# Performance work log

Hardware: AMD Instinct MI355X
Metric: run time of the kernel (lower is better)

The kernel has to match this reference:

```python
import jax, jax.numpy as jnp
import numpy as np

DIM, HEADS, HEAD_DIM, P = 256, 8, 64, 16
N = P * P          # 256 tokens
H2 = HEADS // 2    # heads in SDPA branch
SCALE = HEAD_DIM ** -0.5
BN_EPS = 1e-5


def _depthwise(x, w, kh, kw):
    # x: (b, DIM, P, P), w: (DIM, kh*kw) depthwise kernel -> same spatial size
    rhs = w.reshape(DIM, 1, kh, kw)
    return jax.lax.conv_general_dilated(
        x, rhs, window_strides=(1, 1),
        padding=((kh // 2, kh // 2), (kw // 2, kw // 2)),
        dimension_numbers=('NCHW', 'OIHW', 'NCHW'),
        feature_group_count=DIM)


def setup_inputs() -> dict:
    key = jax.random.key(0)
    ks = jax.random.split(key, 8)
    b = 128
    return {
        'x': jax.random.normal(ks[0], (b, N, DIM), jnp.float32),
        'bn_gamma': jax.random.uniform(ks[1], (DIM,), jnp.float32, 0.5, 1.5),
        'bn_beta': jax.random.normal(ks[2], (DIM,), jnp.float32) * 0.1,
        'bn_mean': jax.random.normal(ks[3], (DIM,), jnp.float32) * 0.1,
        'bn_var': jax.random.uniform(ks[4], (DIM,), jnp.float32, 0.5, 1.5),
        'w_qkv': jax.random.normal(ks[5], (DIM, 6), jnp.float32) * 0.1,
        'w_qs': jax.random.normal(ks[6], (DIM, 3), jnp.float32) * 0.1,
        'w_ks': jax.random.normal(ks[7], (DIM, 3), jnp.float32) * 0.1,
    }


def reference(x, bn_gamma, bn_beta, bn_mean, bn_var, w_qkv, w_qs, w_ks):
    b = x.shape[0]
    # raw contiguous view (b,n,d) -> (b,dim,p,p), as in the torch code
    xi = x.reshape(b, DIM, P, P)
    inv = jax.lax.rsqrt(bn_var + BN_EPS)
    xb = jax.nn.relu(((xi - bn_mean[None, :, None, None]) * (bn_gamma * inv)[None, :, None, None])
                     + bn_beta[None, :, None, None])
    # grouped 1x1 conv (groups=DIM, 6 out-channels per group)
    qkv = (xb[:, :, None, :, :] * w_qkv[None, :, :, None, None]).reshape(b, DIM * 6, P, P)
    # raw view (b, 6*dim, p, p) -> (b, n, 6*dim)
    qkv = qkv.reshape(b, N, 6 * DIM)
    q, k, v = jnp.split(qkv, 3, axis=-1)  # each (b, n, 2*dim)

    def to_heads(t):
        return t.reshape(b, N, HEADS, HEAD_DIM).transpose(0, 2, 1, 3)  # b h n d

    q, k, v = to_heads(q), to_heads(k), to_heads(v)
    q1, k1, v1 = q[:, :H2], k[:, :H2], v[:, :H2]
    # raw reshape (b, H2, n, head_dim) -> (b, dim, p, p)
    q2 = q[:, H2:].reshape(b, DIM, P, P)
    k2 = k[:, H2:].reshape(b, DIM, P, P)
    v2 = v[:, H2:].reshape(b, DIM, P, P)
    q2 = _depthwise(q2, w_qs, 1, 3)
    k2 = _depthwise(k2, w_ks, 3, 1)
    res2 = (q2 + k2 + v2).reshape(b, N, DIM)

    scores = jnp.einsum('bhid,bhjd->bhij', q1, k1) * SCALE
    attn = jax.nn.softmax(scores, axis=-1)
    out = jnp.einsum('bhij,bhjd->bhid', attn, v1)
    out = out.transpose(0, 2, 1, 3).reshape(b, N, H2 * HEAD_DIM)  # (b, n, dim)

    res = jnp.concatenate([out, res2], axis=2)  # (b, n, 2*dim)
    # AdaptiveAvgPool1d(dim) on length 2*dim == pairwise mean
    return res.reshape(b, N, DIM, 2).mean(axis=-1)
```

## Files before the change

### kernel.cpp

```cpp
#include <hip/hip_runtime.h>

typedef __bf16 bf16;
typedef __attribute__((ext_vector_type(8))) __bf16 bf16x8;
typedef __attribute__((ext_vector_type(4))) __bf16 bf16x4;
typedef __attribute__((ext_vector_type(4))) float floatx4;

#define MFMA16(a, b, c) __builtin_amdgcn_mfma_f32_16x16x32_bf16((a), (b), (c), 0, 0, 0)

__device__ __forceinline__ float fast_exp2(float xv) {
#if __has_builtin(__builtin_amdgcn_exp2f)
  return __builtin_amdgcn_exp2f(xv);
#else
  return exp2f(xv);
#endif
}

__global__ __launch_bounds__(256) void attn_kernel(
    const float* __restrict__ x,
    const float* __restrict__ bn_gamma, const float* __restrict__ bn_beta,
    const float* __restrict__ bn_mean, const float* __restrict__ bn_var,
    const float* __restrict__ w_qkv,
    float* __restrict__ out)
{
  __shared__ __align__(16) char smem[65024];
  bf16 (*Abf)[72] = (bf16(*)[72])smem;
  bf16* PstBase   = (bf16*)(smem + 36864);
  bf16 (*Vt)[40]  = (bf16(*)[40])(smem + 57344);
  float* cqA = (float*)(smem + 62464);
  float* ckA = (float*)(smem + 63488);
  bf16*  cvA = (bf16*) (smem + 64512);
  float* scT = (float*)(smem + 36864);
  float* bsT = scT + 256;

  const int t  = threadIdx.x;
  const int bb = blockIdx.x >> 2;
  const int h  = blockIdx.x & 3;

  {
    float inv = rsqrtf(bn_var[t] + 1e-5f);
    float sc  = bn_gamma[t] * inv;
    scT[t] = sc;
    bsT[t] = bn_beta[t] - bn_mean[t] * sc;
    cqA[t] = w_qkv[t*6+0] * (0.125f * 1.44269504088896340736f);
    ckA[t] = w_qkv[t*6+2];
    cvA[t] = (bf16)w_qkv[t*6+4];
  }
  __syncthreads();

  {
    const float* xb = x + ((size_t)bb * 256) * 256 + h * 64;
    const int rsub = t >> 4, ch = t & 15;
#pragma unroll
    for (int it = 0; it < 16; ++it) {
      int n = it*16 + rsub;
      float4 v = *(const float4*)(xb + (size_t)n*256 + ch*4);
      float sc = scT[n], bs = bsT[n];
      bf16x4 bv;
      bv.x = (bf16)fmaxf(fmaf(v.x, sc, bs), 0.f);
      bv.y = (bf16)fmaxf(fmaf(v.y, sc, bs), 0.f);
      bv.z = (bf16)fmaxf(fmaf(v.z, sc, bs), 0.f);
      bv.w = (bf16)fmaxf(fmaf(v.w, sc, bs), 0.f);
      *(bf16x4*)&Abf[n][ch*4] = bv;
    }
  }

  const int lane = t & 63;
  const int wid  = t >> 6;
  const int quad = lane >> 4;
  const int col  = lane & 15;
  const int R    = wid * 64;
  bf16 (*Pst)[40] = (bf16(*)[40])(PstBase + wid * (64*40));

  floatx4 oacc[4][4];
  float lacc[4][4];
  float cqr[4][4];
#pragma unroll
  for (int it = 0; it < 4; ++it)
#pragma unroll
    for (int et = 0; et < 4; ++et)
      oacc[it][et] = (floatx4){0.f,0.f,0.f,0.f};
#pragma unroll
  for (int it = 0; it < 4; ++it)
#pragma unroll
    for (int r = 0; r < 4; ++r) {
      lacc[it][r] = 0.f;
      cqr[it][r]  = cqA[R + it*16 + quad*4 + r];
    }

  for (int jt = 0; jt < 8; ++jt) {
    const int j0 = jt * 32;
    __syncthreads();

#pragma unroll
    for (int qq = 0; qq < 8; ++qq) {
      int q = qq*256 + t;
      int e = q >> 5, jl = q & 31;
      Vt[e][jl] = (bf16)((float)Abf[j0+jl][e] * (float)cvA[j0+jl]);
    }

    bf16x8 bq00 = *(const bf16x8*)&Abf[j0 + col][quad*8];
    bf16x8 bq01 = *(const bf16x8*)&Abf[j0 + col][32 + quad*8];
    bf16x8 bq10 = *(const bf16x8*)&Abf[j0 + 16 + col][quad*8];
    bf16x8 bq11 = *(const bf16x8*)&Abf[j0 + 16 + col][32 + quad*8];
    float ck0 = ckA[j0 + col];
    float ck1 = ckA[j0 + 16 + col];
#pragma unroll
    for (int it = 0; it < 4; ++it) {
      const bf16* arow = &Abf[R + it*16 + col][0];
      bf16x8 a0 = *(const bf16x8*)(arow + quad*8);
      bf16x8 a1 = *(const bf16x8*)(arow + 32 + quad*8);
      floatx4 s0 = (floatx4){0.f,0.f,0.f,0.f};
      floatx4 s1 = (floatx4){0.f,0.f,0.f,0.f};
      s0 = MFMA16(a0, bq00, s0);
      s0 = MFMA16(a1, bq01, s0);
      s1 = MFMA16(a0, bq10, s1);
      s1 = MFMA16(a1, bq11, s1);
#pragma unroll
      for (int r = 0; r < 4; ++r) {
        float p0 = fast_exp2(fminf(cqr[it][r] * ck0 * s0[r], 80.f));
        float p1 = fast_exp2(fminf(cqr[it][r] * ck1 * s1[r], 80.f));
        lacc[it][r] += p0 + p1;
        Pst[it*16 + quad*4 + r][col]      = (bf16)p0;
        Pst[it*16 + quad*4 + r][16 + col] = (bf16)p1;
      }
    }
    __syncthreads();

    bf16x8 vb0 = *(const bf16x8*)&Vt[     col][quad*8];
    bf16x8 vb1 = *(const bf16x8*)&Vt[16 + col][quad*8];
    bf16x8 vb2 = *(const bf16x8*)&Vt[32 + col][quad*8];
    bf16x8 vb3 = *(const bf16x8*)&Vt[48 + col][quad*8];
#pragma unroll
    for (int it = 0; it < 4; ++it) {
      bf16x8 pa = *(const bf16x8*)&Pst[it*16 + col][quad*8];
      oacc[it][0] = MFMA16(pa, vb0, oacc[it][0]);
      oacc[it][1] = MFMA16(pa, vb1, oacc[it][1]);
      oacc[it][2] = MFMA16(pa, vb2, oacc[it][2]);
      oacc[it][3] = MFMA16(pa, vb3, oacc[it][3]);
    }
  }

#pragma unroll
  for (int it = 0; it < 4; ++it)
#pragma unroll
    for (int r = 0; r < 4; ++r) {
      float v = lacc[it][r];
      v += __shfl_xor(v, 1, 64);
      v += __shfl_xor(v, 2, 64);
      v += __shfl_xor(v, 4, 64);
      v += __shfl_xor(v, 8, 64);
      lacc[it][r] = 0.5f / v;
    }

  float* outp = out + ((size_t)bb * 256) * 256 + h * 32;
#pragma unroll
  for (int it = 0; it < 4; ++it)
#pragma unroll
    for (int et = 0; et < 4; ++et)
#pragma unroll
      for (int r = 0; r < 4; ++r) {
        float v  = oacc[it][et][r];
        float v2 = v + __shfl_xor(v, 1, 64);
        if (!(lane & 1)) {
          int n = R + it*16 + quad*4 + r;
          int d = et*8 + (col >> 1);
          outp[(size_t)n*256 + d] = v2 * lacc[it][r];
        }
      }
}

__global__ __launch_bounds__(256) void conv_kernel(
    const float* __restrict__ x,
    const float* __restrict__ bn_gamma, const float* __restrict__ bn_beta,
    const float* __restrict__ bn_mean, const float* __restrict__ bn_var,
    const float* __restrict__ w_qkv, const float* __restrict__ w_qs,
    const float* __restrict__ w_ks,
    float* __restrict__ out)
{
  __shared__ float X[32][68];
  __shared__ float scA[32], bsA[32], wq1[32], wk1[32], wv1[32];
  __shared__ float qs[8][3], ks[8][3];

  const int t     = threadIdx.x;
  const int bb    = blockIdx.x >> 5;
  const int cg    = blockIdx.x & 31;
  const int cbase = cg * 8;
  const int h2    = cbase >> 6;
  const int N0    = (cbase & 63) * 4;

  if (t < 32) {
    int n = N0 + t;
    float inv = rsqrtf(bn_var[n] + 1e-5f);
    float s = bn_gamma[n] * inv;
    scA[t] = s;
    bsA[t] = bn_beta[n] - bn_mean[n] * s;
    wq1[t] = w_qkv[n*6+1];
    wk1[t] = w_qkv[n*6+3];
    wv1[t] = w_qkv[n*6+5];
  } else if (t < 56) {
    int i = t - 32; int cc = i/3, kk = i - cc*3;
    qs[cc][kk] = w_qs[(cbase+cc)*3 + kk];
  } else if (t < 80) {
    int i = t - 56; int cc = i/3, kk = i - cc*3;
    ks[cc][kk] = w_ks[(cbase+cc)*3 + kk];
  }
  __syncthreads();

  {
    const float* src = x + ((size_t)(bb*256 + N0)) * 256 + h2*64;
#pragma unroll
    for (int ii = 0; ii < 2; ++ii) {
      int idx = t + ii*256;
      int row = idx >> 4, ch = idx & 15;
      float4 v = *(const float4*)(src + (size_t)row*256 + ch*4);
      float s = scA[row], b2 = bsA[row];
      X[row][ch*4+0] = fmaxf(fmaf(v.x, s, b2), 0.f);
      X[row][ch*4+1] = fmaxf(fmaf(v.y, s, b2), 0.f);
      X[row][ch*4+2] = fmaxf(fmaf(v.z, s, b2), 0.f);
      X[row][ch*4+3] = fmaxf(fmaf(v.w, s, b2), 0.f);
    }
  }
  __syncthreads();

  const int cc  = t >> 5;
  const int l32 = t & 31;
  float res[4];
#pragma unroll
  for (int k = 0; k < 4; ++k) {
    int u = l32*4 + k;
    float acc = 0.f;
#pragma unroll
    for (int pp = 0; pp < 2; ++pp) {
      int p  = 2*u + pp;
      int ww = p & 15;
      int lr = cc*4 + (p >> 6);
      int e  = p & 63;
      float fc = X[lr][e];
      float qv = qs[cc][1] * fc;
      if (ww > 0)  qv = fmaf(qs[cc][0], X[lr][e-1], qv);
      if (ww < 15) qv = fmaf(qs[cc][2], X[lr][e+1], qv);
      float val = fmaf(qv, wq1[lr], fc * wv1[lr]);
      float kv = ks[cc][1] * fc * wk1[lr];
      if (p >= 16) {
        int pm = p - 16; int lm = cc*4 + (pm >> 6);
        kv = fmaf(ks[cc][0] * wk1[lm], X[lm][pm & 63], kv);
      }
      if (p < 240) {
        int pq = p + 16; int lp = cc*4 + (pq >> 6);
        kv = fmaf(ks[cc][2] * wk1[lp], X[lp][pq & 63], kv);
      }
      acc += val + kv;
    }
    res[k] = 0.5f * acc;
  }
  float4 o4; o4.x = res[0]; o4.y = res[1]; o4.z = res[2]; o4.w = res[3];
  *(float4*)(out + ((size_t)(bb*256 + cbase + cc)) * 256 + 128 + l32*4) = o4;
}

extern "C" void kernel_launch(void* const* d_in, const int* in_sizes, int n_in,
                              void* d_out, int out_size, void* d_ws, size_t ws_size,
                              hipStream_t stream) {
  (void)in_sizes; (void)n_in; (void)out_size; (void)d_ws; (void)ws_size;
  const float* x    = (const float*)d_in[0];
  const float* g    = (const float*)d_in[1];
  const float* be   = (const float*)d_in[2];
  const float* mn   = (const float*)d_in[3];
  const float* vr   = (const float*)d_in[4];
  const float* wqkv = (const float*)d_in[5];
  const float* wqs  = (const float*)d_in[6];
  const float* wks  = (const float*)d_in[7];
  float* out = (float*)d_out;

  attn_kernel<<<dim3(512), dim3(256), 0, stream>>>(x, g, be, mn, vr, wqkv, out);
  conv_kernel<<<dim3(4096), dim3(256), 0, stream>>>(x, g, be, mn, vr, wqkv, wqs, wks, out);
}
```

Measured before the change: 129.0 us.

## Fuse attention and depthwise conv branches into one kernel with register-resident P

Merges the attention and conv kernels into one 512-thread kernel, so each block's BN-normalized bf16 tile of x is reused for the conv branch instead of being reloaded by a separate launch. It folds the v weight into P, keeps P in registers by shuffling it into MFMA operand layout with ds_bpermute instead of staging it in LDS, and double-buffers the V transpose. This removes one launch, the second read of x and the P shared-memory round trip. In exchange the conv branch now reads bf16-rounded inputs, which lowers accuracy, and register pressure under launch_bounds(512,4) may spill.

```diff
diff --git a/kernel.cpp b/kernel.cpp
--- a/kernel.cpp
+++ b/kernel.cpp
@@ -3,9 +3,10 @@
 typedef __bf16 bf16;
 typedef __attribute__((ext_vector_type(8))) __bf16 bf16x8;
 typedef __attribute__((ext_vector_type(4))) __bf16 bf16x4;
+typedef __attribute__((ext_vector_type(2))) __bf16 bf16x2;
 typedef __attribute__((ext_vector_type(4))) float floatx4;
 
-#define MFMA16(a, b, c) __builtin_amdgcn_mfma_f32_16x16x32_bf16((a), (b), (c), 0, 0, 0)
+#define MFMA16(a,b,c) __builtin_amdgcn_mfma_f32_16x16x32_bf16((a),(b),(c),0,0,0)
 
 __device__ __forceinline__ float fast_exp2(float xv) {
 #if __has_builtin(__builtin_amdgcn_exp2f)
@@ -15,44 +16,49 @@
 #endif
 }
 
-__global__ __launch_bounds__(256) void attn_kernel(
+__device__ __forceinline__ void ld8f(const bf16* p, float* dst) {
+  bf16x8 v = *(const bf16x8*)p;
+#pragma unroll
+  for (int i = 0; i < 8; ++i) dst[i] = (float)v[i];
+}
+
+__global__ __launch_bounds__(512, 4) void fused_kernel(
     const float* __restrict__ x,
     const float* __restrict__ bn_gamma, const float* __restrict__ bn_beta,
     const float* __restrict__ bn_mean, const float* __restrict__ bn_var,
-    const float* __restrict__ w_qkv,
+    const float* __restrict__ w_qkv, const float* __restrict__ w_qs,
+    const float* __restrict__ w_ks,
     float* __restrict__ out)
 {
-  __shared__ __align__(16) char smem[65024];
-  bf16 (*Abf)[72] = (bf16(*)[72])smem;
-  bf16* PstBase   = (bf16*)(smem + 36864);
-  bf16 (*Vt)[40]  = (bf16(*)[40])(smem + 57344);
-  float* cqA = (float*)(smem + 62464);
-  float* ckA = (float*)(smem + 63488);
-  bf16*  cvA = (bf16*) (smem + 64512);
+  __shared__ __align__(16) char smem[49152];
+  bf16 (*Abf)[72]    = (bf16(*)[72])smem;
+  bf16 (*Vt)[64][40] = (bf16(*)[64][40])(smem + 36864);
+  float* ckA = (float*)(smem + 47104);
+  float* cvA = (float*)(smem + 48128);
   float* scT = (float*)(smem + 36864);
-  float* bsT = scT + 256;
+  float* bsT = (float*)(smem + 36864 + 1024);
+  float* Lsh = (float*)(smem + 36864);
 
   const int t  = threadIdx.x;
   const int bb = blockIdx.x >> 2;
   const int h  = blockIdx.x & 3;
 
-  {
+  if (t < 256) {
     float inv = rsqrtf(bn_var[t] + 1e-5f);
     float sc  = bn_gamma[t] * inv;
     scT[t] = sc;
     bsT[t] = bn_beta[t] - bn_mean[t] * sc;
-    cqA[t] = w_qkv[t*6+0] * (0.125f * 1.44269504088896340736f);
     ckA[t] = w_qkv[t*6+2];
-    cvA[t] = (bf16)w_qkv[t*6+4];
+    cvA[t] = w_qkv[t*6+4];
   }
   __syncthreads();
 
+  const float* xb = x + (size_t)bb * 65536 + h * 64;
   {
-    const float* xb = x + ((size_t)bb * 256) * 256 + h * 64;
     const int rsub = t >> 4, ch = t & 15;
 #pragma unroll
-    for (int it = 0; it < 16; ++it) {
-      int n = it*16 + rsub;
+    for (int i2 = 0; i2 < 8; ++i2) {
+      int n = i2*32 + rsub;
       float4 v = *(const float4*)(xb + (size_t)n*256 + ch*4);
       float sc = scT[n], bs = bsT[n];
       bf16x4 bv;
@@ -63,198 +69,211 @@
       *(bf16x4*)&Abf[n][ch*4] = bv;
     }
   }
+  __syncthreads();
+
+  {
+    int j = t & 31, g = t >> 5;
+    bf16x4 v = *(const bf16x4*)&Abf[j][g*4];
+    Vt[0][g*4+0][j] = v.x; Vt[0][g*4+1][j] = v.y;
+    Vt[0][g*4+2][j] = v.z; Vt[0][g*4+3][j] = v.w;
+  }
 
   const int lane = t & 63;
   const int wid  = t >> 6;
-  const int quad = lane >> 4;
-  const int col  = lane & 15;
-  const int R    = wid * 64;
-  bf16 (*Pst)[40] = (bf16(*)[40])(PstBase + wid * (64*40));
-
-  floatx4 oacc[4][4];
-  float lacc[4][4];
-  float cqr[4][4];
-#pragma unroll
-  for (int it = 0; it < 4; ++it)
+  const int q    = lane >> 4;
+  const int c    = lane & 15;
+  const int R    = wid * 32;
+  const bool hi  = (q >= 2);
+  const int qa   = q & 1;
+  const int srcA = ((qa*2)*16 + c) * 4;
+  const int srcB = ((qa*2+1)*16 + c) * 4;
+
+  float cqv[2];
+  cqv[0] = w_qkv[(R + c)*6]      * 0.18033688f;
+  cqv[1] = w_qkv[(R + 16 + c)*6] * 0.18033688f;
+
+  floatx4 oacc[2][4];
+  float lacc[2] = {0.f, 0.f};
+#pragma unroll
+  for (int it = 0; it < 2; ++it)
 #pragma unroll
     for (int et = 0; et < 4; ++et)
       oacc[it][et] = (floatx4){0.f,0.f,0.f,0.f};
-#pragma unroll
-  for (int it = 0; it < 4; ++it)
-#pragma unroll
-    for (int r = 0; r < 4; ++r) {
-      lacc[it][r] = 0.f;
-      cqr[it][r]  = cqA[R + it*16 + quad*4 + r];
-    }
 
   for (int jt = 0; jt < 8; ++jt) {
-    const int j0 = jt * 32;
+    const int j0  = jt * 32;
+    const int cur = jt & 1;
     __syncthreads();
 
-#pragma unroll
-    for (int qq = 0; qq < 8; ++qq) {
-      int q = qq*256 + t;
-      int e = q >> 5, jl = q & 31;
-      Vt[e][jl] = (bf16)((float)Abf[j0+jl][e] * (float)cvA[j0+jl]);
-    }
-
-    bf16x8 bq00 = *(const bf16x8*)&Abf[j0 + col][quad*8];
-    bf16x8 bq01 = *(const bf16x8*)&Abf[j0 + col][32 + quad*8];
-    bf16x8 bq10 = *(const bf16x8*)&Abf[j0 + 16 + col][quad*8];
-    bf16x8 bq11 = *(const bf16x8*)&Abf[j0 + 16 + col][32 + quad*8];
-    float ck0 = ckA[j0 + col];
-    float ck1 = ckA[j0 + 16 + col];
-#pragma unroll
-    for (int it = 0; it < 4; ++it) {
-      const bf16* arow = &Abf[R + it*16 + col][0];
-      bf16x8 a0 = *(const bf16x8*)(arow + quad*8);
-      bf16x8 a1 = *(const bf16x8*)(arow + 32 + quad*8);
+    if (jt < 7) {
+      int j = t & 31, g = t >> 5;
+      bf16x4 v = *(const bf16x4*)&Abf[j0 + 32 + j][g*4];
+      Vt[cur^1][g*4+0][j] = v.x; Vt[cur^1][g*4+1][j] = v.y;
+      Vt[cur^1][g*4+2][j] = v.z; Vt[cur^1][g*4+3][j] = v.w;
+    }
+
+    bf16x8 aj00 = *(const bf16x8*)&Abf[j0 + c][8*q];
+    bf16x8 aj01 = *(const bf16x8*)&Abf[j0 + c][32 + 8*q];
+    bf16x8 aj10 = *(const bf16x8*)&Abf[j0 + 16 + c][8*q];
+    bf16x8 aj11 = *(const bf16x8*)&Abf[j0 + 16 + c][32 + 8*q];
+    floatx4 ckv0 = *(const floatx4*)&ckA[j0 + 4*q];
+    floatx4 ckv1 = *(const floatx4*)&ckA[j0 + 16 + 4*q];
+    floatx4 cvv0 = *(const floatx4*)&cvA[j0 + 4*q];
+    floatx4 cvv1 = *(const floatx4*)&cvA[j0 + 16 + 4*q];
+
+    unsigned int paU[2][4];
+#pragma unroll
+    for (int it = 0; it < 2; ++it) {
+      const bf16* bp = &Abf[R + 16*it + c][0];
+      bf16x8 bi0 = *(const bf16x8*)(bp + 8*q);
+      bf16x8 bi1 = *(const bf16x8*)(bp + 32 + 8*q);
       floatx4 s0 = (floatx4){0.f,0.f,0.f,0.f};
       floatx4 s1 = (floatx4){0.f,0.f,0.f,0.f};
-      s0 = MFMA16(a0, bq00, s0);
-      s0 = MFMA16(a1, bq01, s0);
-      s1 = MFMA16(a0, bq10, s1);
-      s1 = MFMA16(a1, bq11, s1);
+      s0 = MFMA16(aj00, bi0, s0); s0 = MFMA16(aj01, bi1, s0);
+      s1 = MFMA16(aj10, bi0, s1); s1 = MFMA16(aj11, bi1, s1);
+      float p0[4], p1[4];
 #pragma unroll
       for (int r = 0; r < 4; ++r) {
-        float p0 = fast_exp2(fminf(cqr[it][r] * ck0 * s0[r], 80.f));
-        float p1 = fast_exp2(fminf(cqr[it][r] * ck1 * s1[r], 80.f));
-        lacc[it][r] += p0 + p1;
-        Pst[it*16 + quad*4 + r][col]      = (bf16)p0;
-        Pst[it*16 + quad*4 + r][16 + col] = (bf16)p1;
+        float e0v = fast_exp2(fminf(cqv[it]*ckv0[r]*s0[r], 80.f));
+        float e1v = fast_exp2(fminf(cqv[it]*ckv1[r]*s1[r], 80.f));
+        lacc[it] += e0v + e1v;
+        p0[r] = e0v * cvv0[r];
+        p1[r] = e1v * cvv1[r];
       }
-    }
-    __syncthreads();
-
-    bf16x8 vb0 = *(const bf16x8*)&Vt[     col][quad*8];
-    bf16x8 vb1 = *(const bf16x8*)&Vt[16 + col][quad*8];
-    bf16x8 vb2 = *(const bf16x8*)&Vt[32 + col][quad*8];
-    bf16x8 vb3 = *(const bf16x8*)&Vt[48 + col][quad*8];
-#pragma unroll
-    for (int it = 0; it < 4; ++it) {
-      bf16x8 pa = *(const bf16x8*)&Pst[it*16 + col][quad*8];
-      oacc[it][0] = MFMA16(pa, vb0, oacc[it][0]);
-      oacc[it][1] = MFMA16(pa, vb1, oacc[it][1]);
-      oacc[it][2] = MFMA16(pa, vb2, oacc[it][2]);
-      oacc[it][3] = MFMA16(pa, vb3, oacc[it][3]);
-    }
-  }
-
-#pragma unroll
-  for (int it = 0; it < 4; ++it)
+      union { bf16x2 hh; unsigned int u; } pk00, pk01, pk10, pk11;
+      pk00.hh = (bf16x2){(bf16)p0[0], (bf16)p0[1]};
+      pk01.hh = (bf16x2){(bf16)p0[2], (bf16)p0[3]};
+      pk10.hh = (bf16x2){(bf16)p1[0], (bf16)p1[1]};
+      pk11.hh = (bf16x2){(bf16)p1[2], (bf16)p1[3]};
+      unsigned int a0, a1;
+      a0 = (unsigned)__builtin_amdgcn_ds_bpermute(srcA, (int)pk00.u);
+      a1 = (unsigned)__builtin_amdgcn_ds_bpermute(srcA, (int)pk10.u);
+      paU[it][0] = hi ? a1 : a0;
+      a0 = (unsigned)__builtin_amdgcn_ds_bpermute(srcA, (int)pk01.u);
+      a1 = (unsigned)__builtin_amdgcn_ds_bpermute(srcA, (int)pk11.u);
+      paU[it][1] = hi ? a1 : a0;
+      a0 = (unsigned)__builtin_amdgcn_ds_bpermute(srcB, (int)pk00.u);
+      a1 = (unsigned)__builtin_amdgcn_ds_bpermute(srcB, (int)pk10.u);
+      paU[it][2] = hi ? a1 : a0;
+      a0 = (unsigned)__builtin_amdgcn_ds_bpermute(srcB, (int)pk01.u);
+      a1 = (unsigned)__builtin_amdgcn_ds_bpermute(srcB, (int)pk11.u);
+      paU[it][3] = hi ? a1 : a0;
+    }
+
+    union PAu { unsigned int u[4]; bf16x8 v; };
+    PAu pa0, pa1;
+#pragma unroll
+    for (int k = 0; k < 4; ++k) { pa0.u[k] = paU[0][k]; pa1.u[k] = paU[1][k]; }
+
+#pragma unroll
+    for (int et = 0; et < 4; ++et) {
+      bf16x8 vb = *(const bf16x8*)&Vt[cur][16*et + c][8*q];
+      oacc[0][et] = MFMA16(pa0.v, vb, oacc[0][et]);
+      oacc[1][et] = MFMA16(pa1.v, vb, oacc[1][et]);
+    }
+  }
+
+  __syncthreads();
+
+#pragma unroll
+  for (int it = 0; it < 2; ++it) {
+    float v = lacc[it];
+    v += __shfl_xor(v, 16, 64);
+    v += __shfl_xor(v, 32, 64);
+    lacc[it] = v;
+  }
+  if (q == 0) {
+    Lsh[R + c]      = lacc[0];
+    Lsh[R + 16 + c] = lacc[1];
+  }
+  floatx4 l40 = *(const floatx4*)&Lsh[R + 4*q];
+  floatx4 l41 = *(const floatx4*)&Lsh[R + 16 + 4*q];
+
+  float* outA = out + ((size_t)bb*256)*256 + h*32;
+#pragma unroll
+  for (int it = 0; it < 2; ++it) {
+    floatx4 l4 = it ? l41 : l40;
 #pragma unroll
     for (int r = 0; r < 4; ++r) {
-      float v = lacc[it][r];
-      v += __shfl_xor(v, 1, 64);
-      v += __shfl_xor(v, 2, 64);
-      v += __shfl_xor(v, 4, 64);
-      v += __shfl_xor(v, 8, 64);
-      lacc[it][r] = 0.5f / v;
-    }
-
-  float* outp = out + ((size_t)bb * 256) * 256 + h * 32;
-#pragma unroll
-  for (int it = 0; it < 4; ++it)
-#pragma unroll
-    for (int et = 0; et < 4; ++et)
-#pragma unroll
-      for (int r = 0; r < 4; ++r) {
-        float v  = oacc[it][et][r];
+      float linv = 0.5f / l4[r];
+      int n = R + 16*it + 4*q + r;
+#pragma unroll
+      for (int et = 0; et < 4; ++et) {
+        float v = oacc[it][et][r];
         float v2 = v + __shfl_xor(v, 1, 64);
-        if (!(lane & 1)) {
-          int n = R + it*16 + quad*4 + r;
-          int d = et*8 + (col >> 1);
-          outp[(size_t)n*256 + d] = v2 * lacc[it][r];
-        }
+        if (!(lane & 1))
+          outA[(size_t)n*256 + 8*et + (c>>1)] = v2 * linv;
       }
-}
-
-__global__ __launch_bounds__(256) void conv_kernel(
-    const float* __restrict__ x,
-    const float* __restrict__ bn_gamma, const float* __restrict__ bn_beta,
-    const float* __restrict__ bn_mean, const float* __restrict__ bn_var,
-    const float* __restrict__ w_qkv, const float* __restrict__ w_qs,
-    const float* __restrict__ w_ks,
-    float* __restrict__ out)
-{
-  __shared__ float X[32][68];
-  __shared__ float scA[32], bsA[32], wq1[32], wk1[32], wv1[32];
-  __shared__ float qs[8][3], ks[8][3];
-
-  const int t     = threadIdx.x;
-  const int bb    = blockIdx.x >> 5;
-  const int cg    = blockIdx.x & 31;
-  const int cbase = cg * 8;
-  const int h2    = cbase >> 6;
-  const int N0    = (cbase & 63) * 4;
-
-  if (t < 32) {
-    int n = N0 + t;
-    float inv = rsqrtf(bn_var[n] + 1e-5f);
-    float s = bn_gamma[n] * inv;
-    scA[t] = s;
-    bsA[t] = bn_beta[n] - bn_mean[n] * s;
-    wq1[t] = w_qkv[n*6+1];
-    wk1[t] = w_qkv[n*6+3];
-    wv1[t] = w_qkv[n*6+5];
-  } else if (t < 56) {
-    int i = t - 32; int cc = i/3, kk = i - cc*3;
-    qs[cc][kk] = w_qs[(cbase+cc)*3 + kk];
-  } else if (t < 80) {
-    int i = t - 56; int cc = i/3, kk = i - cc*3;
-    ks[cc][kk] = w_ks[(cbase+cc)*3 + kk];
-  }
-  __syncthreads();
+    }
+  }
 
   {
-    const float* src = x + ((size_t)(bb*256 + N0)) * 256 + h2*64;
-#pragma unroll
-    for (int ii = 0; ii < 2; ++ii) {
-      int idx = t + ii*256;
-      int row = idx >> 4, ch = idx & 15;
-      float4 v = *(const float4*)(src + (size_t)row*256 + ch*4);
-      float s = scA[row], b2 = bsA[row];
-      X[row][ch*4+0] = fmaxf(fmaf(v.x, s, b2), 0.f);
-      X[row][ch*4+1] = fmaxf(fmaf(v.y, s, b2), 0.f);
-      X[row][ch*4+2] = fmaxf(fmaf(v.z, s, b2), 0.f);
-      X[row][ch*4+3] = fmaxf(fmaf(v.w, s, b2), 0.f);
-    }
-  }
-  __syncthreads();
-
-  const int cc  = t >> 5;
-  const int l32 = t & 31;
-  float res[4];
-#pragma unroll
-  for (int k = 0; k < 4; ++k) {
-    int u = l32*4 + k;
-    float acc = 0.f;
-#pragma unroll
-    for (int pp = 0; pp < 2; ++pp) {
-      int p  = 2*u + pp;
-      int ww = p & 15;
-      int lr = cc*4 + (p >> 6);
-      int e  = p & 63;
-      float fc = X[lr][e];
-      float qv = qs[cc][1] * fc;
-      if (ww > 0)  qv = fmaf(qs[cc][0], X[lr][e-1], qv);
-      if (ww < 15) qv = fmaf(qs[cc][2], X[lr][e+1], qv);
-      float val = fmaf(qv, wq1[lr], fc * wv1[lr]);
-      float kv = ks[cc][1] * fc * wk1[lr];
-      if (p >= 16) {
-        int pm = p - 16; int lm = cc*4 + (pm >> 6);
-        kv = fmaf(ks[cc][0] * wk1[lm], X[lm][pm & 63], kv);
-      }
-      if (p < 240) {
-        int pq = p + 16; int lp = cc*4 + (pq >> 6);
-        kv = fmaf(ks[cc][2] * wk1[lp], X[lp][pq & 63], kv);
-      }
-      acc += val + kv;
-    }
-    res[k] = 0.5f * acc;
-  }
-  float4 o4; o4.x = res[0]; o4.y = res[1]; o4.z = res[2]; o4.w = res[3];
-  *(float4*)(out + ((size_t)(bb*256 + cbase + cc)) * 256 + 128 + l32*4) = o4;
+    const int ci = t >> 3, sub = t & 7, qq = sub >> 1, uh = sub & 1;
+    const int C  = h*64 + ci;
+    const int a  = 4*ci + qq;
+    const int e0 = 32*uh;
+
+    float qs0 = w_qs[C*3+0], qs1 = w_qs[C*3+1], qs2 = w_qs[C*3+2];
+    float ks0 = w_ks[C*3+0], ks1 = w_ks[C*3+1], ks2 = w_ks[C*3+2];
+    float wq1a = w_qkv[a*6+1], wk1a = w_qkv[a*6+3], wv1a = w_qkv[a*6+5];
+    float wcf = fmaf(ks1, wk1a, wv1a);
+
+    float wmx = 0.f;
+    if (uh) wmx = ks0 * wk1a;
+    else if (qq > 0) wmx = ks0 * w_qkv[(a-1)*6+3];
+    float wmh = ks0 * wk1a;
+    float wpl = ks2 * wk1a;
+    float wpx = 0.f;
+    if (!uh) wpx = ks2 * wk1a;
+    else if (qq < 3) wpx = ks2 * w_qkv[(a+1)*6+3];
+
+    float Xc[32], Xl[16], Xr[16];
+#pragma unroll
+    for (int m = 0; m < 4; ++m) ld8f(&Abf[a][e0 + 8*m], &Xc[8*m]);
+    if (uh) {
+      ld8f(&Abf[a][16], &Xl[0]); ld8f(&Abf[a][24], &Xl[8]);
+    } else if (qq > 0) {
+      ld8f(&Abf[a-1][48], &Xl[0]); ld8f(&Abf[a-1][56], &Xl[8]);
+    } else {
+#pragma unroll
+      for (int i = 0; i < 16; ++i) Xl[i] = 0.f;
+    }
+    if (!uh) {
+      ld8f(&Abf[a][32], &Xr[0]); ld8f(&Abf[a][40], &Xr[8]);
+    } else if (qq < 3) {
+      ld8f(&Abf[a+1][0], &Xr[0]); ld8f(&Abf[a+1][8], &Xr[8]);
+    } else {
+#pragma unroll
+      for (int i = 0; i < 16; ++i) Xr[i] = 0.f;
+    }
+
+    float res[16];
+    float prev = 0.f;
+#pragma unroll
+    for (int k = 0; k < 32; ++k) {
+      float fc = Xc[k];
+      float qv = qs1 * fc;
+      if (k & 15)         qv = fmaf(qs0, Xc[k-1], qv);
+      if ((k & 15) != 15) qv = fmaf(qs2, Xc[k+1], qv);
+      float acc = fmaf(wq1a, qv, wcf * fc);
+      float tm = (k < 16) ? Xl[k]     : Xc[k-16];
+      float wm = (k < 16) ? wmx       : wmh;
+      acc = fmaf(wm, tm, acc);
+      float tp = (k < 16) ? Xc[k+16]  : Xr[k-16];
+      float wp = (k < 16) ? wpl       : wpx;
+      acc = fmaf(wp, tp, acc);
+      if (k & 1) res[k>>1] = 0.5f * (prev + acc);
+      else       prev = acc;
+    }
+
+    float* outC = out + ((size_t)(bb*256 + C))*256 + 128 + 32*qq + 16*uh;
+#pragma unroll
+    for (int m = 0; m < 4; ++m) {
+      float4 o4;
+      o4.x = res[4*m]; o4.y = res[4*m+1]; o4.z = res[4*m+2]; o4.w = res[4*m+3];
+      *(float4*)(outC + 4*m) = o4;
+    }
+  }
 }
 
 extern "C" void kernel_launch(void* const* d_in, const int* in_sizes, int n_in,
@@ -271,6 +290,5 @@
   const float* wks  = (const float*)d_in[7];
   float* out = (float*)d_out;
 
-  attn_kernel<<<dim3(512), dim3(256), 0, stream>>>(x, g, be, mn, vr, wqkv, out);
-  conv_kernel<<<dim3(4096), dim3(256), 0, stream>>>(x, g, be, mn, vr, wqkv, wqs, wks, out);
-}
+  fused_kernel<<<dim3(512), dim3(512), 0, stream>>>(x, g, be, mn, vr, wqkv, wqs, wks, out);
+}
```

New measurement: 113.8 us. 1.13x faster.
